# Performance work log

Measured on AMD Instinct MI355X. Metric: run time of the kernel, lower is better.

The kernel has to match this reference:

```python
import jax, jax.numpy as jnp
import numpy as np

P, L, H = 3, 4, 6          # window size, num scales, num heads
EPS = 1e-5                 # LayerNorm eps (PyTorch default)


def setup_inputs() -> dict:
    key = jax.random.key(0)
    B, T, D = 8, 4096, 768
    ks = jax.random.split(key, 12)
    s = 0.02
    w = lambda k, shape: (jax.random.normal(k, shape, jnp.float32) * s)
    z = lambda n: jnp.zeros((n,), jnp.float32)
    return {
        "x": jax.random.normal(ks[0], (B, T, D), jnp.float32),
        "ln_g": jnp.ones((D,), jnp.float32),
        "ln_b": z(D),
        "qw": w(ks[1], (D, D)), "qb": z(D),
        "kw": w(ks[2], (D, D)), "kb": z(D),
        "vw": w(ks[3], (D, D)), "vb": z(D),
        "inw": w(ks[4], (3 * D, D)), "inb": z(3 * D),   # MHA in_proj
        "mow": w(ks[5], (D, D)), "mob": z(D),            # MHA out_proj
        "ow": w(ks[6], (D, D)), "ob": z(D),              # output_proj
    }


def _layernorm(x, g, b):
    mu = jnp.mean(x, -1, keepdims=True)
    var = jnp.mean((x - mu) ** 2, -1, keepdims=True)
    return (x - mu) * jax.lax.rsqrt(var + EPS) * g + b


def _mha_windows(q, k, v, inw, inb, mow, mob):
    # q,k,v: [B, W, P, D] -- batched tiny attention over all windows at once
    B, W, Pw, D = q.shape
    hd = D // H
    wq, wk, wv = inw[:D], inw[D:2 * D], inw[2 * D:]
    bq, bk, bv = inb[:D], inb[D:2 * D], inb[2 * D:]
    qp = (q @ wq.T + bq).reshape(B, W, Pw, H, hd)
    kp = (k @ wk.T + bk).reshape(B, W, Pw, H, hd)
    vp = (v @ wv.T + bv).reshape(B, W, Pw, H, hd)
    scores = jnp.einsum('bwqhd,bwkhd->bwhqk', qp, kp) / jnp.sqrt(jnp.float32(hd))
    attn = jax.nn.softmax(scores, axis=-1)
    o = jnp.einsum('bwhqk,bwkhd->bwqhd', attn, vp).reshape(B, W, Pw, D)
    return o @ mow.T + mob


def reference(x, ln_g, ln_b, qw, qb, kw, kb, vw, vb, inw, inb, mow, mob, ow, ob):
    B, T, D = x.shape
    xn = _layernorm(x, ln_g, ln_b)
    Q = xn @ qw.T + qb
    K = xn @ kw.T + kb
    V = xn @ vw.T + vb
    acc = jnp.zeros_like(x)
    for kk in range(L):
        scale = P ** kk
        if T < scale:
            continue
        Lp = T // scale
        pool = lambda z: z[:, :Lp * scale].reshape(B, Lp, scale, D).mean(axis=2)
        pQ, pK, pV = pool(Q), pool(K), pool(V)
        W = Lp // P
        if W == 0:
            continue
        win = lambda z: z[:, :W * P].reshape(B, W, P, D)
        o = _mha_windows(win(pQ), win(pK), win(pV), inw, inb, mow, mob)
        so = o.reshape(B, W * P, D)                       # concat of windows
        idx = (jnp.arange(T) * (W * P)) // T              # nearest interp to T
        up = so[:, idx]
        acc = acc + jax.nn.gelu(up, approximate=False)    # exact GELU (torch default)
    out = acc @ ow.T + ob
    return x + out
```

## Files before the change

### kernel.cpp

```cpp
#include <hip/hip_runtime.h>
#include <stdint.h>

typedef short s16x8 __attribute__((ext_vector_type(8)));
typedef float f32x4 __attribute__((ext_vector_type(4)));

__device__ __forceinline__ unsigned short f2bf(float f) {
  unsigned u = __builtin_bit_cast(unsigned, f);
  u = (u + 0x7FFFu + ((u >> 16) & 1u)) >> 16;
  return (unsigned short)u;
}
__device__ __forceinline__ float bf2f(unsigned short h) {
  unsigned u = ((unsigned)h) << 16;
  return __builtin_bit_cast(float, u);
}

__device__ __forceinline__ void gload_lds16(const void* g, void* l) {
  __builtin_amdgcn_global_load_lds((__attribute__((address_space(1))) void*)g,
                                   (__attribute__((address_space(3))) void*)l,
                                   16, 0, 0);
}

__global__ __launch_bounds__(256)
void mstr_convw(const float* __restrict__ inw, const float* __restrict__ mow,
                const float* __restrict__ ow, unsigned short* __restrict__ inwB,
                unsigned short* __restrict__ mowB, unsigned short* __restrict__ owB)
{
  long i = (long)blockIdx.x * 256 + threadIdx.x;
  const long n1 = 589824;
  if (i < 3 * n1)      inwB[i] = f2bf(inw[i]);
  else if (i < 4 * n1) mowB[i - 3 * n1] = f2bf(mow[i - 3 * n1]);
  else                 owB[i - 4 * n1] = f2bf(ow[i - 4 * n1]);
}

__global__ __launch_bounds__(256)
void mstr_transpose(const float* __restrict__ qw, const float* __restrict__ kw,
                    const float* __restrict__ vw, unsigned short* __restrict__ wT)
{
  const float* src = (blockIdx.z == 0) ? qw : (blockIdx.z == 1) ? kw : vw;
  unsigned short* dst = wT + (long)blockIdx.z * 589824;
  __shared__ float tile[32][33];
  int tx = threadIdx.x & 31, ty = threadIdx.x >> 5;
  int j0 = blockIdx.x * 32, k0 = blockIdx.y * 32;
#pragma unroll
  for (int i = 0; i < 4; ++i)
    tile[ty + i * 8][tx] = src[(long)(j0 + ty + i * 8) * 768 + k0 + tx];
  __syncthreads();
#pragma unroll
  for (int i = 0; i < 4; ++i)
    dst[(long)(k0 + ty + i * 8) * 768 + j0 + tx] = f2bf(tile[tx][ty + i * 8]);
}

__global__ __launch_bounds__(256)
void mstr_biascomb(const float* __restrict__ inw, const float* __restrict__ inb,
                   const float* __restrict__ qb, const float* __restrict__ kb,
                   const float* __restrict__ vb, float* __restrict__ bc,
                   float* __restrict__ zb)
{
  int gid = blockIdx.x * 256 + threadIdx.x;
  if (gid < 768) zb[gid] = 0.f;
  int s = gid / 768, c = gid - s * 768;
  const float* b = (s == 0) ? qb : (s == 1) ? kb : vb;
  const float* wrow = inw + (long)(s * 768 + c) * 768;
  float a = inb[s * 768 + c];
  for (int j = 0; j < 768; ++j) a += b[j] * wrow[j];
  bc[gid] = a;
}

__global__ __launch_bounds__(256)
void mstr_ln(const float* __restrict__ x, const float* __restrict__ g,
             const float* __restrict__ bt, unsigned short* __restrict__ xn)
{
  int blk = blockIdx.x;
  int bb = blk / 4095, t = blk - bb * 4095;
  const float* xr = x + ((long)bb * 4096 + t) * 768;
  unsigned short* orow = xn + (long)blk * 768;
  int tid = threadIdx.x;
  float v0 = xr[tid], v1 = xr[tid + 256], v2 = xr[tid + 512];
  float s = v0 + v1 + v2;
  float s2 = v0 * v0 + v1 * v1 + v2 * v2;
#pragma unroll
  for (int o = 32; o > 0; o >>= 1) { s += __shfl_down(s, o, 64); s2 += __shfl_down(s2, o, 64); }
  __shared__ float rs[4], rq[4];
  int lane = tid & 63, wid = tid >> 6;
  if (lane == 0) { rs[wid] = s; rq[wid] = s2; }
  __syncthreads();
  float S = rs[0] + rs[1] + rs[2] + rs[3];
  float S2 = rq[0] + rq[1] + rq[2] + rq[3];
  float mu = S * (1.0f / 768.0f);
  float var = S2 * (1.0f / 768.0f) - mu * mu;
  float rstd = rsqrtf(var + 1e-5f);
  orow[tid] = f2bf((v0 - mu) * rstd * g[tid] + bt[tid]);
  orow[tid + 256] = f2bf((v1 - mu) * rstd * g[tid + 256] + bt[tid + 256]);
  orow[tid + 512] = f2bf((v2 - mu) * rstd * g[tid + 512] + bt[tid + 512]);
}

template<int EPI>
__global__ __launch_bounds__(256, 4)
void mstr_gemm(const unsigned short* __restrict__ A, int M,
               const unsigned short* __restrict__ W,
               const float* __restrict__ bias,
               unsigned short* out0, unsigned short* out1, unsigned short* out2,
               float* outf, const float* xadd,
               int rowDiv, int rowStride, int NC, int nwg)
{
  __shared__ char smem[49152];
  int orig = blockIdx.x;
  int swq = nwg >> 3, swr = nwg & 7;
  int xcd = orig & 7, sidx = orig >> 3;
  int wg = (xcd < swr ? xcd * (swq + 1) : swr * (swq + 1) + (xcd - swr) * swq) + sidx;
  int rowp = wg / NC, colp = wg - rowp * NC;

  const int tid = threadIdx.x;
  const int lane = tid & 63;
  const int wid = tid >> 6;
  const int wr = wid >> 1, wc = wid & 1;
  const long row0 = (long)rowp * 128;
  const int col0 = colp * 128;

  const int sr = tid >> 2;
  const int sc = (((tid & 3) ^ ((tid >> 3) & 3)) << 3);
  long a0r = row0 + sr;       if (a0r >= M) a0r = M - 1;
  long a1r = row0 + sr + 64;  if (a1r >= M) a1r = M - 1;
  const unsigned short* Ag0 = A + a0r * 768 + sc;
  const unsigned short* Ag1 = A + a1r * 768 + sc;
  const unsigned short* Bg0 = W + (long)(col0 + sr) * 768 + sc;
  const unsigned short* Bg1 = W + (long)(col0 + sr + 64) * 768 + sc;
  char* ldsT = smem + tid * 16;

  const int fr = lane & 15;
  const int g4 = lane >> 4;
  const int cx = ((g4 ^ ((fr >> 1) & 3)) << 4);
  const int aoff = (wr * 64 + fr) * 64 + cx;
  const int boff = 8192 + (wc * 64 + fr) * 64 + cx;

  f32x4 acc[4][4] = {};

#define MSTAGE(T, BO) { int kk_ = (T) * 32; \
    gload_lds16(Ag0 + kk_, ldsT + (BO)); \
    gload_lds16(Ag1 + kk_, ldsT + (BO) + 4096); \
    gload_lds16(Bg0 + kk_, ldsT + (BO) + 8192); \
    gload_lds16(Bg1 + kk_, ldsT + (BO) + 12288); }

  MSTAGE(0, 0)
  int stBo = 16384;
  int rdBo = 0;
  for (int t = 0; t < 24; ++t) {
    if (t < 23) {
      MSTAGE(t + 1, stBo)
      stBo += 16384; if (stBo == 49152) stBo = 0;
      asm volatile("s_waitcnt vmcnt(4)" ::: "memory");
    } else {
      asm volatile("s_waitcnt vmcnt(0)" ::: "memory");
    }
    __builtin_amdgcn_s_barrier();
    const int bo = rdBo;
    rdBo += 16384; if (rdBo == 49152) rdBo = 0;
    s16x8 af[4], bfv[4];
#pragma unroll
    for (int m = 0; m < 4; ++m) af[m] = *(const s16x8*)(smem + bo + aoff + m * 1024);
#pragma unroll
    for (int n = 0; n < 4; ++n) bfv[n] = *(const s16x8*)(smem + bo + boff + n * 1024);
    __builtin_amdgcn_s_setprio(1);
#pragma unroll
    for (int m = 0; m < 4; ++m)
#pragma unroll
      for (int n = 0; n < 4; ++n)
        acc[m][n] = __builtin_amdgcn_mfma_f32_16x16x32_bf16(af[m], bfv[n], acc[m][n], 0, 0, 0);
    __builtin_amdgcn_s_setprio(0);
  }
#undef MSTAGE

  int seg = (col0 >= 1536) ? 2 : (col0 >= 768 ? 1 : 0);
  unsigned short* outp = (seg == 0) ? out0 : (seg == 1) ? out1 : out2;
  int csub = seg * 768;
#pragma unroll
  for (int m = 0; m < 4; ++m) {
#pragma unroll
    for (int r = 0; r < 4; ++r) {
      long gr = row0 + wr * 64 + m * 16 + g4 * 4 + r;
      if (gr < M) {
        long orow;
        if (EPI == 1) {
          orow = gr;
        } else {
          int qq = (int)gr / rowDiv;
          orow = (long)qq * rowStride + ((int)gr - qq * rowDiv);
        }
#pragma unroll
        for (int n = 0; n < 4; ++n) {
          int c = col0 + wc * 64 + n * 16 + fr;
          float v = acc[m][n][r] + bias[c];
          if (EPI == 1) {
            long o = gr * 768 + c;
            outf[o] = v + xadd[o];
          } else if (EPI == 2) {
            v = 0.5f * v * (1.0f + erff(v * 0.70710678118654752f));
            outp[orow * 768 + (c - csub)] = f2bf(v);
          } else {
            outp[orow * 768 + (c - csub)] = f2bf(v);
          }
        }
      }
    }
  }
}

__global__ __launch_bounds__(384)
void mstr_pool(unsigned short* qp, unsigned short* kp, unsigned short* vp,
               int srcOff, int dstOff, int Ndst)
{
  unsigned short* p = (blockIdx.y == 0) ? qp : (blockIdx.y == 1) ? kp : vp;
  int tok = blockIdx.x;
  int bb = tok / Ndst, j = tok - bb * Ndst;
  long sb = ((long)bb * 6063 + srcOff + 3 * j) * 768 + threadIdx.x * 2;
  long db = ((long)bb * 6063 + dstOff + j) * 768 + threadIdx.x * 2;
  unsigned a = *(const unsigned*)(p + sb);
  unsigned b = *(const unsigned*)(p + sb + 768);
  unsigned c = *(const unsigned*)(p + sb + 1536);
  float lo = (bf2f((unsigned short)a) + bf2f((unsigned short)b) + bf2f((unsigned short)c)) * (1.0f / 3.0f);
  float hi = (bf2f((unsigned short)(a >> 16)) + bf2f((unsigned short)(b >> 16)) + bf2f((unsigned short)(c >> 16))) * (1.0f / 3.0f);
  unsigned o = (unsigned)f2bf(lo) | ((unsigned)f2bf(hi) << 16);
  *(unsigned*)(p + db) = o;
}

__global__ __launch_bounds__(256)
void mstr_attn(unsigned short* qp, unsigned short* kp, unsigned short* vp, int nwaves)
{
  int gw = blockIdx.x * 4 + (threadIdx.x >> 6);
  if (gw >= nwaves) return;
  int lane = threadIdx.x & 63;
  int win = gw / 6, h = gw - win * 6;
  int bb = win / 2021, ww = win - bb * 2021;
  int row0;
  if (ww < 1365)      row0 = 3 * ww;
  else if (ww < 1820) row0 = 4095 + 3 * (ww - 1365);
  else if (ww < 1971) row0 = 5460 + 3 * (ww - 1820);
  else                row0 = 5913 + 3 * (ww - 1971);
  long base = ((long)bb * 6063 + row0) * 768 + h * 128 + lane * 2;
  float q[3][2], k[3][2], v[3][2];
#pragma unroll
  for (int i = 0; i < 3; ++i) {
    unsigned uq = *(const unsigned*)(qp + base + i * 768);
    unsigned uk = *(const unsigned*)(kp + base + i * 768);
    unsigned uv = *(const unsigned*)(vp + base + i * 768);
    q[i][0] = bf2f((unsigned short)uq); q[i][1] = bf2f((unsigned short)(uq >> 16));
    k[i][0] = bf2f((unsigned short)uk); k[i][1] = bf2f((unsigned short)(uk >> 16));
    v[i][0] = bf2f((unsigned short)uv); v[i][1] = bf2f((unsigned short)(uv >> 16));
  }
  float s[3][3];
#pragma unroll
  for (int i = 0; i < 3; ++i)
#pragma unroll
    for (int j = 0; j < 3; ++j)
      s[i][j] = q[i][0] * k[j][0] + q[i][1] * k[j][1];
#pragma unroll
  for (int st = 1; st < 64; st <<= 1) {
#pragma unroll
    for (int i = 0; i < 3; ++i)
#pragma unroll
      for (int j = 0; j < 3; ++j)
        s[i][j] += __shfl_xor(s[i][j], st, 64);
  }
  const float scl = 0.088388347648318447f;
#pragma unroll
  for (int i = 0; i < 3; ++i) {
    float s0 = s[i][0] * scl, s1 = s[i][1] * scl, s2 = s[i][2] * scl;
    float m = fmaxf(s0, fmaxf(s1, s2));
    float e0 = __expf(s0 - m), e1 = __expf(s1 - m), e2 = __expf(s2 - m);
    float inv = 1.0f / (e0 + e1 + e2);
    e0 *= inv; e1 *= inv; e2 *= inv;
    float o0 = e0 * v[0][0] + e1 * v[1][0] + e2 * v[2][0];
    float o1 = e0 * v[0][1] + e1 * v[1][1] + e2 * v[2][1];
    unsigned o = (unsigned)f2bf(o0) | ((unsigned)f2bf(o1) << 16);
    *(unsigned*)(qp + base + i * 768) = o;
  }
}

__global__ __launch_bounds__(256)
void mstr_gelusum(const unsigned short* __restrict__ omo, unsigned short* __restrict__ acc)
{
  long gid = (long)blockIdx.x * 256 + threadIdx.x;
  int d2 = (int)(gid % 384);
  long row = gid / 384;
  int bb = (int)(row >> 12);
  int t = (int)(row & 4095);
  const int NkA[4] = {4095, 1365, 453, 150};
  const int soA[4] = {0, 4095, 5460, 5913};
  float a0 = 0.f, a1 = 0.f;
#pragma unroll
  for (int kk = 0; kk < 4; ++kk) {
    int idx = (t * NkA[kk]) >> 12;
    long tok = (long)bb * 6063 + soA[kk] + idx;
    unsigned u = *(const unsigned*)(omo + tok * 768 + d2 * 2);
    a0 += bf2f((unsigned short)u);
    a1 += bf2f((unsigned short)(u >> 16));
  }
  unsigned o = (unsigned)f2bf(a0) | ((unsigned)f2bf(a1) << 16);
  *(unsigned*)(acc + row * 768 + d2 * 2) = o;
}

extern "C" void kernel_launch(void* const* d_in, const int* in_sizes, int n_in,
                              void* d_out, int out_size, void* d_ws, size_t ws_size,
                              hipStream_t stream)
{
  const float* x   = (const float*)d_in[0];
  const float* lng = (const float*)d_in[1];
  const float* lnb = (const float*)d_in[2];
  const float* qw  = (const float*)d_in[3];
  const float* qb  = (const float*)d_in[4];
  const float* kw  = (const float*)d_in[5];
  const float* kb  = (const float*)d_in[6];
  const float* vw  = (const float*)d_in[7];
  const float* vb  = (const float*)d_in[8];
  const float* inw = (const float*)d_in[9];
  const float* inb = (const float*)d_in[10];
  const float* mob = (const float*)d_in[12];
  const float* ow  = (const float*)d_in[13];
  const float* ob  = (const float*)d_in[14];

  const long n1 = 589824;
  char* ws = (char*)d_ws;
  size_t off = 0;
  auto alloc = [&](size_t bytes) -> char* {
    char* p = ws + off;
    off += (bytes + 255) & ~(size_t)255;
    return p;
  };
  unsigned short* Wc = (unsigned short*)alloc((size_t)5 * n1 * 2);
  float* bc = (float*)alloc(2304 * 4);
  float* zb = (float*)alloc(768 * 4);
  size_t fixed = off;

  int g = 0;
  const int cands[4] = {8, 4, 2, 1};
  for (int ci = 0; ci < 4; ++ci) {
    int c = cands[ci];
    size_t need = fixed + (size_t)c * 4096 * 768 * 2
                + 2 * (size_t)c * 6063 * 768 * 2
                + 1024;
    if (need <= ws_size) { g = c; break; }
  }
  if (!g) return;

  char* GR = ws + fixed;
  unsigned short* xnacc = (unsigned short*)GR;
  unsigned short* qp = xnacc + (size_t)g * 4096 * 768;
  unsigned short* kp = qp + (size_t)g * 6063 * 768;
  unsigned short* inwB = (unsigned short*)GR;
  unsigned short* wT   = inwB + 3 * n1;

  unsigned short* mowB = Wc + 3 * n1;
  unsigned short* owB  = Wc + 4 * n1;

  mstr_convw<<<dim3(11520), dim3(256), 0, stream>>>(inw, (const float*)d_in[11], ow, inwB, mowB, owB);
  mstr_transpose<<<dim3(24, 24, 3), dim3(256), 0, stream>>>(qw, kw, vw, wT);
  mstr_biascomb<<<dim3(9), dim3(256), 0, stream>>>(inw, inb, qb, kb, vb, bc, zb);
  for (int s = 0; s < 3; ++s)
    mstr_gemm<0><<<dim3(36), dim3(256), 0, stream>>>(inwB + (long)s * n1, 768, wT + (long)s * n1,
                                                     zb, Wc + (long)s * n1, Wc + (long)s * n1,
                                                     Wc + (long)s * n1, nullptr, nullptr, 768, 768, 6, 36);

  int ng = 8 / g;
  for (int gi = 0; gi < ng; ++gi) {
    const float* xg = x + (long)gi * g * 4096 * 768;
    unsigned short* vp = (unsigned short*)d_out + (long)gi * g * 4096 * 768 * 2;
    mstr_ln<<<dim3(g * 4095), dim3(256), 0, stream>>>(xg, lng, lnb, xnacc);
    int M1 = g * 4095, gb1 = (M1 + 127) / 128;
    int nwg1 = gb1 * 18;
    mstr_gemm<0><<<dim3(nwg1), dim3(256), 0, stream>>>(xnacc, M1, Wc, bc,
                                                       qp, kp, vp, nullptr, nullptr,
                                                       4095, 6063, 18, nwg1);
    mstr_pool<<<dim3(g * 1365, 3), dim3(384), 0, stream>>>(qp, kp, vp, 0, 4095, 1365);
    mstr_pool<<<dim3(g * 453, 3), dim3(384), 0, stream>>>(qp, kp, vp, 4095, 5460, 453);
    mstr_pool<<<dim3(g * 150, 3), dim3(384), 0, stream>>>(qp, kp, vp, 5460, 5913, 150);
    int nw = g * 2021 * 6;
    mstr_attn<<<dim3((nw + 3) / 4), dim3(256), 0, stream>>>(qp, kp, vp, nw);
    int M2 = g * 6063;
    int nwg2 = ((M2 + 127) / 128) * 6;
    mstr_gemm<2><<<dim3(nwg2), dim3(256), 0, stream>>>(qp, M2, mowB, mob, kp, kp, kp,
                                                       nullptr, nullptr, M2, 0, 6, nwg2);
    mstr_gelusum<<<dim3(g * 6144), dim3(256), 0, stream>>>(kp, xnacc);
    int M3 = g * 4096;
    int nwg3 = (M3 / 128) * 6;
    mstr_gemm<1><<<dim3(nwg3), dim3(256), 0, stream>>>(xnacc, M3, owB, ob, nullptr, nullptr, nullptr,
                                                       (float*)d_out + (long)gi * g * 4096 * 768, xg,
                                                       M3, 0, 6, nwg3);
  }
}
```

Measured before the change: 627.0 us.

## Switch GEMM to 32x32x16 MFMA with double-buffered LDS

Replaces the 16x16x32 bf16 MFMA tiling with 32x32x16 MFMA instructions, so each wave computes four 32x32 accumulators. This reduces LDS fragment reads per MFMA and the instruction count. The triple-buffered LDS pipeline with explicit vmcnt waits becomes double buffering with a __syncthreads after each k-step, cutting LDS to 32KB. The trade-off is less latency hiding: every iteration now ends in a full barrier, and the prefetch is only one stage ahead.

```diff
diff --git a/kernel.cpp b/kernel.cpp
--- a/kernel.cpp
+++ b/kernel.cpp
@@ -2,7 +2,7 @@
 #include <stdint.h>
 
 typedef short s16x8 __attribute__((ext_vector_type(8)));
-typedef float f32x4 __attribute__((ext_vector_type(4)));
+typedef float f32x16 __attribute__((ext_vector_type(16)));
 
 __device__ __forceinline__ unsigned short f2bf(float f) {
   unsigned u = __builtin_bit_cast(unsigned, f);
@@ -103,7 +103,7 @@
                float* outf, const float* xadd,
                int rowDiv, int rowStride, int NC, int nwg)
 {
-  __shared__ char smem[49152];
+  __shared__ char smem[32768];
   int orig = blockIdx.x;
   int swq = nwg >> 3, swr = nwg & 7;
   int xcd = orig & 7, sidx = orig >> 3;
@@ -113,7 +113,7 @@
   const int tid = threadIdx.x;
   const int lane = tid & 63;
   const int wid = tid >> 6;
-  const int wr = wid >> 1, wc = wid & 1;
+  const int wm = wid >> 1, wn = wid & 1;
   const long row0 = (long)rowp * 128;
   const int col0 = colp * 128;
 
@@ -121,88 +121,85 @@
   const int sc = (((tid & 3) ^ ((tid >> 3) & 3)) << 3);
   long a0r = row0 + sr;       if (a0r >= M) a0r = M - 1;
   long a1r = row0 + sr + 64;  if (a1r >= M) a1r = M - 1;
-  const unsigned short* Ag0 = A + a0r * 768 + sc;
-  const unsigned short* Ag1 = A + a1r * 768 + sc;
-  const unsigned short* Bg0 = W + (long)(col0 + sr) * 768 + sc;
-  const unsigned short* Bg1 = W + (long)(col0 + sr + 64) * 768 + sc;
-  char* ldsT = smem + tid * 16;
-
-  const int fr = lane & 15;
-  const int g4 = lane >> 4;
-  const int cx = ((g4 ^ ((fr >> 1) & 3)) << 4);
-  const int aoff = (wr * 64 + fr) * 64 + cx;
-  const int boff = 8192 + (wc * 64 + fr) * 64 + cx;
-
-  f32x4 acc[4][4] = {};
-
-#define MSTAGE(T, BO) { int kk_ = (T) * 32; \
-    gload_lds16(Ag0 + kk_, ldsT + (BO)); \
-    gload_lds16(Ag1 + kk_, ldsT + (BO) + 4096); \
-    gload_lds16(Bg0 + kk_, ldsT + (BO) + 8192); \
-    gload_lds16(Bg1 + kk_, ldsT + (BO) + 12288); }
+  const unsigned short* pa0 = A + a0r * 768 + sc;
+  const unsigned short* pa1 = A + a1r * 768 + sc;
+  const unsigned short* pb0 = W + (long)(col0 + sr) * 768 + sc;
+  const unsigned short* pb1 = W + (long)(col0 + sr + 64) * 768 + sc;
+
+  const int l5 = lane >> 5;
+  const int rl = lane & 31;
+  const int key = (lane >> 1) & 3;
+  const int aoff = (wm * 64 + rl) * 64 + ((l5 ^ key) << 4);
+  const int boff = 8192 + (wn * 64 + rl) * 64 + ((l5 ^ key) << 4);
+  const int aoffX = aoff ^ 32;
+  const int boffX = boff ^ 32;
+
+  f32x16 acc00 = {}, acc01 = {}, acc10 = {}, acc11 = {};
+
+#define MSTAGE(T, BO) { long ko = (long)(T) * 32; \
+    gload_lds16(pa0 + ko, smem + (BO) + tid * 16); \
+    gload_lds16(pa1 + ko, smem + (BO) + 4096 + tid * 16); \
+    gload_lds16(pb0 + ko, smem + (BO) + 8192 + tid * 16); \
+    gload_lds16(pb1 + ko, smem + (BO) + 12288 + tid * 16); }
 
   MSTAGE(0, 0)
-  int stBo = 16384;
-  int rdBo = 0;
+  __syncthreads();
+
   for (int t = 0; t < 24; ++t) {
-    if (t < 23) {
-      MSTAGE(t + 1, stBo)
-      stBo += 16384; if (stBo == 49152) stBo = 0;
-      asm volatile("s_waitcnt vmcnt(4)" ::: "memory");
-    } else {
-      asm volatile("s_waitcnt vmcnt(0)" ::: "memory");
-    }
-    __builtin_amdgcn_s_barrier();
-    const int bo = rdBo;
-    rdBo += 16384; if (rdBo == 49152) rdBo = 0;
-    s16x8 af[4], bfv[4];
-#pragma unroll
-    for (int m = 0; m < 4; ++m) af[m] = *(const s16x8*)(smem + bo + aoff + m * 1024);
-#pragma unroll
-    for (int n = 0; n < 4; ++n) bfv[n] = *(const s16x8*)(smem + bo + boff + n * 1024);
+    const int bo = (t & 1) << 14;
+    if (t < 23) MSTAGE(t + 1, bo ^ 16384)
+    const char* sb = smem + bo;
+    s16x8 a00 = *(const s16x8*)(sb + aoff);
+    s16x8 a01 = *(const s16x8*)(sb + aoffX);
+    s16x8 a10 = *(const s16x8*)(sb + aoff + 2048);
+    s16x8 a11 = *(const s16x8*)(sb + aoffX + 2048);
+    s16x8 b00 = *(const s16x8*)(sb + boff);
+    s16x8 b01 = *(const s16x8*)(sb + boffX);
+    s16x8 b10 = *(const s16x8*)(sb + boff + 2048);
+    s16x8 b11 = *(const s16x8*)(sb + boffX + 2048);
     __builtin_amdgcn_s_setprio(1);
-#pragma unroll
-    for (int m = 0; m < 4; ++m)
-#pragma unroll
-      for (int n = 0; n < 4; ++n)
-        acc[m][n] = __builtin_amdgcn_mfma_f32_16x16x32_bf16(af[m], bfv[n], acc[m][n], 0, 0, 0);
+    acc00 = __builtin_amdgcn_mfma_f32_32x32x16_bf16(a00, b00, acc00, 0, 0, 0);
+    acc00 = __builtin_amdgcn_mfma_f32_32x32x16_bf16(a01, b01, acc00, 0, 0, 0);
+    acc01 = __builtin_amdgcn_mfma_f32_32x32x16_bf16(a00, b10, acc01, 0, 0, 0);
+    acc01 = __builtin_amdgcn_mfma_f32_32x32x16_bf16(a01, b11, acc01, 0, 0, 0);
+    acc10 = __builtin_amdgcn_mfma_f32_32x32x16_bf16(a10, b00, acc10, 0, 0, 0);
+    acc10 = __builtin_amdgcn_mfma_f32_32x32x16_bf16(a11, b01, acc10, 0, 0, 0);
+    acc11 = __builtin_amdgcn_mfma_f32_32x32x16_bf16(a10, b10, acc11, 0, 0, 0);
+    acc11 = __builtin_amdgcn_mfma_f32_32x32x16_bf16(a11, b11, acc11, 0, 0, 0);
     __builtin_amdgcn_s_setprio(0);
+    __syncthreads();
   }
 #undef MSTAGE
 
   int seg = (col0 >= 1536) ? 2 : (col0 >= 768 ? 1 : 0);
   unsigned short* outp = (seg == 0) ? out0 : (seg == 1) ? out1 : out2;
   int csub = seg * 768;
-#pragma unroll
-  for (int m = 0; m < 4; ++m) {
-#pragma unroll
-    for (int r = 0; r < 4; ++r) {
-      long gr = row0 + wr * 64 + m * 16 + g4 * 4 + r;
-      if (gr < M) {
-        long orow;
-        if (EPI == 1) {
-          orow = gr;
-        } else {
-          int qq = (int)gr / rowDiv;
-          orow = (long)qq * rowStride + ((int)gr - qq * rowDiv);
-        }
-#pragma unroll
-        for (int n = 0; n < 4; ++n) {
-          int c = col0 + wc * 64 + n * 16 + fr;
-          float v = acc[m][n][r] + bias[c];
-          if (EPI == 1) {
-            long o = gr * 768 + c;
-            outf[o] = v + xadd[o];
-          } else if (EPI == 2) {
-            v = 0.5f * v * (1.0f + erff(v * 0.70710678118654752f));
-            outp[orow * 768 + (c - csub)] = f2bf(v);
-          } else {
-            outp[orow * 768 + (c - csub)] = f2bf(v);
-          }
-        }
-      }
-    }
-  }
+
+#define EPIW(ACC, MB, NB) { \
+    int c = col0 + wn * 64 + (NB) * 32 + rl; \
+    float bv = bias[c]; \
+    _Pragma("unroll") \
+    for (int reg = 0; reg < 16; ++reg) { \
+      long gr = row0 + wm * 64 + (MB) * 32 + (reg & 3) + 8 * (reg >> 2) + 4 * l5; \
+      if (gr < M) { \
+        float v = ACC[reg] + bv; \
+        if (EPI == 1) { \
+          long o = gr * 768 + c; \
+          outf[o] = v + xadd[o]; \
+        } else { \
+          int qq = (int)gr / rowDiv; \
+          long orow = (long)qq * rowStride + ((int)gr - qq * rowDiv); \
+          if (EPI == 2) v = 0.5f * v * (1.0f + erff(v * 0.70710678118654752f)); \
+          outp[orow * 768 + (c - csub)] = f2bf(v); \
+        } \
+      } \
+    } }
+
+  EPIW(acc00, 0, 0)
+  EPIW(acc01, 0, 1)
+  EPIW(acc10, 1, 0)
+  EPIW(acc11, 1, 1)
+#undef EPIW
 }
 
 __global__ __launch_bounds__(384)
```

New measurement: 735.3 us. 1.17x slower.
